# Kernel optimization log

Hardware: AMD Instinct MI355X
Metric: run time of the kernel (lower is better)

The kernel has to match this reference:

```python
import jax, jax.numpy as jnp
import numpy as np

B, D_IN, H, D_OUT = 4096, 64, 128, 512
MAX_STEP = 1000


def setup_inputs() -> dict:
    key = jax.random.key(0)
    ks = jax.random.split(key, 6)
    return {
        "LT": jax.random.uniform(ks[0], (B, D_IN), jnp.float32),
        "K": jax.random.uniform(ks[1], (D_IN, H), jnp.float32),
        "AT": jax.random.uniform(ks[2], (H,), jnp.float32),
        "u": jax.random.uniform(ks[3], (D_IN * H, D_OUT), jnp.float32),
        "e": jax.random.uniform(ks[4], (H, D_OUT), jnp.float32),
        "b": jax.random.uniform(ks[5], (D_OUT,), jnp.float32),
        "max_step": MAX_STEP,
    }


def _st_relu(x):
    # _mask: relu forward, identity backward (straight-through)
    return x + jax.lax.stop_gradient(jax.nn.relu(x) - x)


def _fixed_point(LT, K, AT, max_step):
    # Competitive-binding fixed point. All quantities here are detached in the
    # original (K.detach(), AT.detach()); callers pass stop_gradient'ed values.
    Bn, Din = LT.shape
    Hn = AT.shape[0]
    LTe = LT[:, :, None]            # [B, D_in, 1]
    ATe = AT[:, None]               # [H, 1] broadcasts against [B, H, 1]
    AF0 = jnp.zeros((Bn, Hn, 1), LT.dtype)
    LF0 = jnp.zeros((Bn, Din, 1), LT.dtype)

    def cond(c):
        AF, LF, step, done = c
        return (step < max_step) & (~done)

    def body(c):
        AF, LF, step, _ = c
        Ldi = LTe / (K @ AF + 1.0)            # [B, D_in, 1]
        AF_new = ATe / (K.T @ Ldi + 1.0)      # [B, H, 1]
        Adi = ATe / (K.T @ LF + 1.0)          # [B, H, 1]
        LF_new = LTe / (K @ Adi + 1.0)        # [B, D_in, 1]
        diff = (jnp.abs(AF_new - AF) / (AF + 1e-5)).max() + \
               (jnp.abs(LF_new - LF) / (LF + 1e-5)).max()
        return AF_new, LF_new, step + 1, diff < 1e-3

    AF, LF, _, _ = jax.lax.while_loop(
        cond, body, (AF0, LF0, jnp.int32(0), jnp.array(False)))
    return AF, LF


def reference(LT, K, AT, u, e, b, max_step):
    Km = _st_relu(K)
    ATm = _st_relu(AT)
    sg = jax.lax.stop_gradient
    AF, LF = _fixed_point(sg(LT), sg(Km), sg(ATm), max_step)

    # Final (differentiable) refinement step with undetached params
    LTe = LT[:, :, None]
    ATe = ATm[:, None]
    Ldi = LTe / (Km @ AF + 1.0)
    AF = ATe / (Km.T @ Ldi + 1.0)             # [B, H, 1]
    Adi = ATe / (Km.T @ LF + 1.0)
    LF = LTe / (Km @ Adi + 1.0)               # [B, D_in, 1]

    AFt = jnp.transpose(AF, (0, 2, 1))        # [B, 1, H]
    D = (Km * (LF @ AFt)).reshape(LT.shape[0], -1)  # [B, D_in*H]
    AFs = AFt[:, 0, :]                        # [B, H]
    return D @ u + AFs @ e + b[None, :]       # [B, D_out]
```

## Files before the change

kernel.cpp:

```cpp
#include <hip/hip_runtime.h>

#define B_ROWS 4096
#define DIN 64
#define NH 128
#define DOUT 512
#define ROWS_PER_BLK 16
#define MAXSTEP_CAP 1000

typedef __attribute__((ext_vector_type(8))) short short8;
typedef __attribute__((ext_vector_type(4))) float f32x4;
typedef __attribute__((ext_vector_type(4))) unsigned u32x4;

template<int N> struct IC { static constexpr int v = N; };

__device__ inline unsigned bf16pair(float lo, float hi) {
    unsigned a = __float_as_uint(lo), b = __float_as_uint(hi);
    a = (a + 0x7fffu + ((a >> 16) & 1u)) >> 16;
    b = (b + 0x7fffu + ((b >> 16) & 1u)) >> 16;
    return a | (b << 16);
}
__device__ inline ushort bf16r(float v) {
    unsigned u = __float_as_uint(v);
    return (ushort)((u + 0x7fffu + ((u >> 16) & 1u)) >> 16);
}
__device__ inline float frcp(float x) { return __builtin_amdgcn_rcpf(x); }
__device__ inline short8 as_s8(u32x4 v) { return __builtin_bit_cast(short8, v); }

__device__ inline void splitw(float v, ushort* ph, ushort* pl) {
    unsigned u = __float_as_uint(v);
    unsigned uh = (u + 0x7fffu + ((u >> 16) & 1u)) & 0xffff0000u;
    float rs = v - __uint_as_float(uh);
    unsigned ul = __float_as_uint(rs);
    *ph = (ushort)(uh >> 16);
    *pl = (ushort)((ul + 0x7fffu + ((ul >> 16) & 1u)) >> 16);
}
__device__ inline void packsplit8(const float* x, short8& h8, short8& l8) {
    unsigned hb[8], lb[8];
    #pragma unroll
    for (int j = 0; j < 8; ++j) {
        float v = fmaxf(x[j], 0.0f);
        unsigned u = __float_as_uint(v);
        unsigned uh = (u + 0x7fffu + ((u >> 16) & 1u)) & 0xffff0000u;
        float rs = v - __uint_as_float(uh);
        unsigned ul = __float_as_uint(rs);
        hb[j] = uh >> 16;
        lb[j] = (ul + 0x7fffu + ((ul >> 16) & 1u)) >> 16;
    }
    uint4 hv, lv;
    hv.x = hb[0] | (hb[1] << 16); hv.y = hb[2] | (hb[3] << 16);
    hv.z = hb[4] | (hb[5] << 16); hv.w = hb[6] | (hb[7] << 16);
    lv.x = lb[0] | (lb[1] << 16); lv.y = lb[2] | (lb[3] << 16);
    lv.z = lb[4] | (lb[5] << 16); lv.w = lb[6] | (lb[7] << 16);
    h8 = *reinterpret_cast<short8*>(&hv);
    l8 = *reinterpret_cast<short8*>(&lv);
}

#define ISSUE_SLICE(buf, ptr) do {                                                         \
    const char* _p = (ptr);                                                                \
    asm volatile("global_load_dwordx4 %0, %1, off"             : "=v"(buf[0]) : "v"(_p));  \
    asm volatile("global_load_dwordx4 %0, %1, off offset:1024" : "=v"(buf[1]) : "v"(_p));  \
    asm volatile("global_load_dwordx4 %0, %1, off offset:2048" : "=v"(buf[2]) : "v"(_p));  \
    asm volatile("global_load_dwordx4 %0, %1, off offset:3072" : "=v"(buf[3]) : "v"(_p));  \
} while (0)

#define WAIT_VM(N) do {                                  \
    asm volatile("s_waitcnt vmcnt(" #N ")");             \
    __builtin_amdgcn_sched_barrier(0);                   \
} while (0)

__global__ __launch_bounds__(256, 1)
void solve_chain(const float* __restrict__ LT, const float* __restrict__ Kg,
                 const float* __restrict__ AT, const int* __restrict__ msp,
                 float* __restrict__ AFout, float* __restrict__ LFout)
{
    __shared__ __align__(16) ushort AX[2][16][136];
    __shared__ __align__(16) ushort AY[2][16][136];
    __shared__ __align__(16) ushort LX[2][16][136];
    __shared__ __align__(16) ushort LY[2][16][136];
    __shared__ float wred[4];

    const int tid = threadIdx.x;
    const int lane = tid & 63, w = tid >> 6;
    const int lr = lane & 15, lg = lane >> 4;
    const int b0row = blockIdx.x * ROWS_PER_BLK;

    for (int idx = tid; idx < 2176; idx += 256) {
        reinterpret_cast<unsigned*>(&AX[0][0][0])[idx] = 0u;
        reinterpret_cast<unsigned*>(&LX[0][0][0])[idx] = 0u;
    }

    int max_step = *msp;
    if (max_step > MAXSTEP_CAP) max_step = MAXSTEP_CAP;

    short8 BkH[4], BkL[4];
    #pragma unroll
    for (int ks = 0; ks < 4; ++ks) {
        float xx[8];
        const float* p = &Kg[(16 * w + lr) * NH + ks * 32 + lg * 8];
        #pragma unroll
        for (int j = 0; j < 8; ++j) xx[j] = p[j];
        packsplit8(xx, BkH[ks], BkL[ks]);
    }
    short8 BtH[2][2], BtL[2][2];
    #pragma unroll
    for (int t = 0; t < 2; ++t)
        #pragma unroll
        for (int ks = 0; ks < 2; ++ks) {
            float xx[8];
            #pragma unroll
            for (int j = 0; j < 8; ++j)
                xx[j] = Kg[(ks * 32 + lg * 8 + j) * NH + 32 * w + 16 * t + lr];
            packsplit8(xx, BtH[t][ks], BtL[t][ks]);
        }

    float ltv[4];
    #pragma unroll
    for (int r = 0; r < 4; ++r)
        ltv[r] = LT[(size_t)(b0row + lg * 4 + r) * DIN + 16 * w + lr];
    float atv[2];
    #pragma unroll
    for (int t = 0; t < 2; ++t)
        atv[t] = fmaxf(AT[32 * w + 16 * t + lr], 0.f);

    float prevA[2][4] = {};
    float prevL[4] = {};
    bool done = false;

    __syncthreads();

    auto iterate = [&](auto MC, bool check, float tol) {
        constexpr int mode = decltype(MC)::v;
        {
            f32x4 aH = {0.f,0.f,0.f,0.f}, aL = aH;
            #pragma unroll
            for (int ks = 0; ks < 4; ++ks) {
                short8 hi = *reinterpret_cast<const short8*>(&AX[0][lr][ks * 32 + lg * 8]);
                aH = __builtin_amdgcn_mfma_f32_16x16x32_bf16(hi, BkH[ks], aH, 0, 0, 0);
                if (mode >= 1) {
                    short8 lo = *reinterpret_cast<const short8*>(&AX[1][lr][ks * 32 + lg * 8]);
                    aL = __builtin_amdgcn_mfma_f32_16x16x32_bf16(lo, BkH[ks], aL, 0, 0, 0);
                }
                if (mode == 2)
                    aL = __builtin_amdgcn_mfma_f32_16x16x32_bf16(hi, BkL[ks], aL, 0, 0, 0);
            }
            #pragma unroll
            for (int r = 0; r < 4; ++r) {
                float v = ltv[r] * frcp(aH[r] + aL[r] + 1.0f);
                if (mode == 0) AY[0][lg * 4 + r][16 * w + lr] = bf16r(v);
                else splitw(v, &AY[0][lg * 4 + r][16 * w + lr],
                               &AY[1][lg * 4 + r][16 * w + lr]);
            }
        }
        {
            short8 xh0 = *reinterpret_cast<const short8*>(&LX[0][lr][lg * 8]);
            short8 xh1 = *reinterpret_cast<const short8*>(&LX[0][lr][32 + lg * 8]);
            short8 xl0, xl1;
            if (mode >= 1) {
                xl0 = *reinterpret_cast<const short8*>(&LX[1][lr][lg * 8]);
                xl1 = *reinterpret_cast<const short8*>(&LX[1][lr][32 + lg * 8]);
            }
            #pragma unroll
            for (int t = 0; t < 2; ++t) {
                f32x4 bH = {0.f,0.f,0.f,0.f}, bL = bH;
                bH = __builtin_amdgcn_mfma_f32_16x16x32_bf16(xh0, BtH[t][0], bH, 0, 0, 0);
                bH = __builtin_amdgcn_mfma_f32_16x16x32_bf16(xh1, BtH[t][1], bH, 0, 0, 0);
                if (mode >= 1) {
                    bL = __builtin_amdgcn_mfma_f32_16x16x32_bf16(xl0, BtH[t][0], bL, 0, 0, 0);
                    bL = __builtin_amdgcn_mfma_f32_16x16x32_bf16(xl1, BtH[t][1], bL, 0, 0, 0);
                }
                if (mode == 2) {
                    bL = __builtin_amdgcn_mfma_f32_16x16x32_bf16(xh0, BtL[t][0], bL, 0, 0, 0);
                    bL = __builtin_amdgcn_mfma_f32_16x16x32_bf16(xh1, BtL[t][1], bL, 0, 0, 0);
                }
                #pragma unroll
                for (int r = 0; r < 4; ++r) {
                    float v = atv[t] * frcp(bH[r] + bL[r] + 1.0f);
                    if (mode == 0) LY[0][lg * 4 + r][32 * w + 16 * t + lr] = bf16r(v);
                    else splitw(v, &LY[0][lg * 4 + r][32 * w + 16 * t + lr],
                                   &LY[1][lg * 4 + r][32 * w + 16 * t + lr]);
                }
            }
        }
        __syncthreads();
        float flag = -1.0f;
        {
            short8 yh0 = *reinterpret_cast<const short8*>(&AY[0][lr][lg * 8]);
            short8 yh1 = *reinterpret_cast<const short8*>(&AY[0][lr][32 + lg * 8]);
            short8 yl0, yl1;
            if (mode >= 1) {
                yl0 = *reinterpret_cast<const short8*>(&AY[1][lr][lg * 8]);
                yl1 = *reinterpret_cast<const short8*>(&AY[1][lr][32 + lg * 8]);
            }
            #pragma unroll
            for (int t = 0; t < 2; ++t) {
                f32x4 bH = {0.f,0.f,0.f,0.f}, bL = bH;
                bH = __builtin_amdgcn_mfma_f32_16x16x32_bf16(yh0, BtH[t][0], bH, 0, 0, 0);
                bH = __builtin_amdgcn_mfma_f32_16x16x32_bf16(yh1, BtH[t][1], bH, 0, 0, 0);
                if (mode >= 1) {
                    bL = __builtin_amdgcn_mfma_f32_16x16x32_bf16(yl0, BtH[t][0], bL, 0, 0, 0);
                    bL = __builtin_amdgcn_mfma_f32_16x16x32_bf16(yl1, BtH[t][1], bL, 0, 0, 0);
                }
                if (mode == 2) {
                    bL = __builtin_amdgcn_mfma_f32_16x16x32_bf16(yh0, BtL[t][0], bL, 0, 0, 0);
                    bL = __builtin_amdgcn_mfma_f32_16x16x32_bf16(yh1, BtL[t][1], bL, 0, 0, 0);
                }
                #pragma unroll
                for (int r = 0; r < 4; ++r) {
                    float v = atv[t] * frcp(bH[r] + bL[r] + 1.0f);
                    if (check) {
                        float p = prevA[t][r];
                        flag = fmaxf(flag, fabsf(v - p) - tol * (p + 1e-5f));
                    }
                    prevA[t][r] = v;
                    if (mode == 0) AX[0][lg * 4 + r][32 * w + 16 * t + lr] = bf16r(v);
                    else splitw(v, &AX[0][lg * 4 + r][32 * w + 16 * t + lr],
                                   &AX[1][lg * 4 + r][32 * w + 16 * t + lr]);
                }
            }
        }
        {
            f32x4 aH = {0.f,0.f,0.f,0.f}, aL = aH;
            #pragma unroll
            for (int ks = 0; ks < 4; ++ks) {
                short8 hi = *reinterpret_cast<const short8*>(&LY[0][lr][ks * 32 + lg * 8]);
                aH = __builtin_amdgcn_mfma_f32_16x16x32_bf16(hi, BkH[ks], aH, 0, 0, 0);
                if (mode >= 1) {
                    short8 lo = *reinterpret_cast<const short8*>(&LY[1][lr][ks * 32 + lg * 8]);
                    aL = __builtin_amdgcn_mfma_f32_16x16x32_bf16(lo, BkH[ks], aL, 0, 0, 0);
                }
                if (mode == 2)
                    aL = __builtin_amdgcn_mfma_f32_16x16x32_bf16(hi, BkL[ks], aL, 0, 0, 0);
            }
            #pragma unroll
            for (int r = 0; r < 4; ++r) {
                float v = ltv[r] * frcp(aH[r] + aL[r] + 1.0f);
                if (check) {
                    float p = prevL[r];
                    flag = fmaxf(flag, fabsf(v - p) - tol * (p + 1e-5f));
                }
                prevL[r] = v;
                if (mode == 0) LX[0][lg * 4 + r][16 * w + lr] = bf16r(v);
                else splitw(v, &LX[0][lg * 4 + r][16 * w + lr],
                               &LX[1][lg * 4 + r][16 * w + lr]);
            }
        }
        if (check) {
            #pragma unroll
            for (int off = 32; off; off >>= 1)
                flag = fmaxf(flag, __shfl_xor(flag, off));
            if (lane == 0) wred[w] = flag;
        }
        __syncthreads();
        if (check)
            done = fmaxf(fmaxf(wred[0], wred[1]), fmaxf(wred[2], wred[3])) < 0.0f;
    };

    int step = 0;
    const int cheapN = max_step < 12 ? max_step : 12;
    for (int s = 0; s < cheapN; ++s, ++step)
        iterate(IC<0>{}, false, 0.f);
    const int capC = max_step < 64 ? max_step : 64;
    while (step < capC && !done) { iterate(IC<0>{}, true, 6e-3f); ++step; }
    done = false;
    while (step < max_step && !done) { iterate(IC<1>{}, true, 5e-5f); ++step; }
    iterate(IC<2>{}, false, 0.f);
    iterate(IC<2>{}, false, 0.f);
    iterate(IC<2>{}, false, 0.f);

    #pragma unroll
    for (int t = 0; t < 2; ++t)
        #pragma unroll
        for (int r = 0; r < 4; ++r)
            AFout[(size_t)(b0row + lg * 4 + r) * NH + 32 * w + 16 * t + lr] = prevA[t][r];
    #pragma unroll
    for (int r = 0; r < 4; ++r)
        LFout[(size_t)(b0row + lg * 4 + r) * DIN + 16 * w + lr] = prevL[r];
}

__global__ __launch_bounds__(256, 2)
void prep_wt2(const float* __restrict__ Kg, const float* __restrict__ ug,
              const float* __restrict__ eg, ushort* __restrict__ WT2)
{
    __shared__ float tile[128][68];
    const int t = threadIdx.x;
    const int i = blockIdx.x;
    const int ot = blockIdx.y;
    const int k0 = i * 128;
    const bool mn = (i < 64);

    {
        const int r = t >> 1, c0 = (t & 1) * 32;
        const float* src = mn ? &ug[(size_t)(k0 + r) * DOUT + ot * 64 + c0]
                              : &eg[(size_t)r * DOUT + ot * 64 + c0];
        const float sc = mn ? fmaxf(Kg[k0 + r], 0.0f) : 1.0f;
        #pragma unroll
        for (int g = 0; g < 8; ++g) {
            float4 v = *reinterpret_cast<const float4*>(src + g * 4);
            v.x *= sc; v.y *= sc; v.z *= sc; v.w *= sc;
            *reinterpret_cast<float4*>(&tile[r][c0 + g * 4]) = v;
        }
    }
    __syncthreads();

    {
        const int wnf = t >> 4;
        const int f = wnf & 7;
        const int wn = wnf >> 3;
        const int ks = f & 3, n = (f >> 2) & 1;
        ushort* dst = WT2 + ((size_t)(ot * 65 + i) * 16 + wnf) * 512;
        #pragma unroll
        for (int q = 0; q < 4; ++q) {
            const int l = (t & 15) * 4 + q;
            const int rb = ks * 32 + (l >> 4) * 8;
            const int c  = wn * 32 + n * 16 + (l & 15);
            uint4 v;
            v.x = bf16pair(tile[rb + 0][c], tile[rb + 1][c]);
            v.y = bf16pair(tile[rb + 2][c], tile[rb + 3][c]);
            v.z = bf16pair(tile[rb + 4][c], tile[rb + 5][c]);
            v.w = bf16pair(tile[rb + 6][c], tile[rb + 7][c]);
            *reinterpret_cast<uint4*>(dst + l * 8) = v;
        }
    }
}

__global__ __launch_bounds__(256, 2)
void out_gemm_rank1(const float* __restrict__ AFw, const float* __restrict__ LFw,
                    const ushort* __restrict__ WT2, const float* __restrict__ bg,
                    float* __restrict__ out)
{
    __shared__ __align__(16) ushort AFb[64][136];
    __shared__ __align__(16) float  LFt[64][68];

    const int t = threadIdx.x;
    const int ot = blockIdx.x & 7;
    const int b0 = (blockIdx.x >> 3) * 64, o0 = ot * 64;
    const int w = t >> 6, l = t & 63;
    const int lr = l & 15, lg = l >> 4;

    {
        const int row = t >> 2, q = t & 3;
        const float4* srcA = reinterpret_cast<const float4*>(
            &AFw[(size_t)(b0 + row) * NH + q * 32]);
        #pragma unroll
        for (int g = 0; g < 4; ++g) {
            float4 fa = srcA[2 * g], fb = srcA[2 * g + 1];
            uint4 wv;
            wv.x = bf16pair(fa.x, fa.y); wv.y = bf16pair(fa.z, fa.w);
            wv.z = bf16pair(fb.x, fb.y); wv.w = bf16pair(fb.z, fb.w);
            *reinterpret_cast<uint4*>(&AFb[row][q * 32 + g * 8]) = wv;
        }
        const f32x4* srcL = reinterpret_cast<const f32x4*>(
            &LFw[(size_t)(b0 + row) * DIN + q * 16]);
        #pragma unroll
        for (int g = 0; g < 4; ++g) {
            f32x4 fv = srcL[g];
            #pragma unroll
            for (int j = 0; j < 4; ++j)
                LFt[q * 16 + g * 4 + j][row] = fv[j];
        }
    }
    __syncthreads();

    const char* base = reinterpret_cast<const char*>(WT2)
        + ((size_t)(ot * 65) * 16) * 1024 + w * 4096 + l * 16;

    u32x4 bf0[4], bf1[4], bf2[4];
    ISSUE_SLICE(bf0, base);
    ISSUE_SLICE(bf1, base + 16384);
    ISSUE_SLICE(bf2, base + 2 * 16384);

    short8 afr[4][4];
    #pragma unroll
    for (int m = 0; m < 4; ++m)
        #pragma unroll
        for (int ks = 0; ks < 4; ++ks)
            afr[m][ks] = *reinterpret_cast<const short8*>(
                &AFb[m * 16 + lr][ks * 32 + lg * 8]);

    f32x4 acc[4], tt[4];
    #pragma unroll
    for (int m = 0; m < 4; ++m) acc[m] = (f32x4){0.f, 0.f, 0.f, 0.f};

    auto computeI = [&](const u32x4* bf) {
        #pragma unroll
        for (int m = 0; m < 4; ++m) tt[m] = (f32x4){0.f, 0.f, 0.f, 0.f};
        #pragma unroll
        for (int ks = 0; ks < 4; ++ks) {
            short8 bv = as_s8(bf[ks]);
            #pragma unroll
            for (int m = 0; m < 4; ++m)
                tt[m] = __builtin_amdgcn_mfma_f32_16x16x32_bf16(afr[m][ks], bv, tt[m], 0, 0, 0);
        }
    };
    auto scaleAdd = [&](int i) {
        #pragma unroll
        for (int m = 0; m < 4; ++m) {
            f32x4 lf = *reinterpret_cast<const f32x4*>(&LFt[i][m * 16 + lg * 4]);
            #pragma unroll
            for (int r = 0; r < 4; ++r)
                acc[m][r] += lf[r] * tt[m][r];
        }
    };

    #pragma unroll 1
    for (int i = 0; i < 60; i += 3) {
        const char* p = base + (size_t)(i + 3) * 16384;
        WAIT_VM(8); computeI(bf0); scaleAdd(i);     ISSUE_SLICE(bf0, p);
        WAIT_VM(8); computeI(bf1); scaleAdd(i + 1); ISSUE_SLICE(bf1, p + 16384);
        WAIT_VM(8); computeI(bf2); scaleAdd(i + 2); ISSUE_SLICE(bf2, p + 2 * 16384);
    }
    WAIT_VM(8); computeI(bf0); scaleAdd(60); ISSUE_SLICE(bf0, base + (size_t)63 * 16384);
    WAIT_VM(8); computeI(bf1); scaleAdd(61); ISSUE_SLICE(bf1, base + (size_t)64 * 16384);
    WAIT_VM(8); computeI(bf2); scaleAdd(62);
    WAIT_VM(4); computeI(bf0); scaleAdd(63);
    WAIT_VM(0); computeI(bf1);
    #pragma unroll
    for (int m = 0; m < 4; ++m)
        #pragma unroll
        for (int r = 0; r < 4; ++r)
            acc[m][r] += tt[m][r];

    const int col = o0 + w * 16 + lr;
    const float bb = bg[col];
    #pragma unroll
    for (int m = 0; m < 4; ++m) {
        #pragma unroll
        for (int r = 0; r < 4; ++r) {
            const int row = b0 + m * 16 + lg * 4 + r;
            out[(size_t)row * DOUT + col] = acc[m][r] + bb;
        }
    }
}

extern "C" void kernel_launch(void* const* d_in, const int* in_sizes, int n_in,
                              void* d_out, int out_size, void* d_ws, size_t ws_size,
                              hipStream_t stream)
{
    const float* LT   = (const float*)d_in[0];
    const float* Kg   = (const float*)d_in[1];
    const float* AT   = (const float*)d_in[2];
    const float* ug   = (const float*)d_in[3];
    const float* eg   = (const float*)d_in[4];
    const float* bg   = (const float*)d_in[5];
    const int*   msp  = (const int*)d_in[6];
    float* out = (float*)d_out;

    char* ws = (char*)d_ws;
    float*  AFw = (float*)(ws);
    float*  LFw = (float*)(ws + 2097152);
    ushort* WT2 = (ushort*)(ws + 3145728);

    solve_chain<<<dim3(256), dim3(256), 0, stream>>>(LT, Kg, AT, msp, AFw, LFw);
    prep_wt2<<<dim3(65, 8), dim3(256), 0, stream>>>(Kg, ug, eg, WT2);

    out_gemm_rank1<<<dim3(512), dim3(256), 0, stream>>>(AFw, LFw, WT2, bg, out);
}
```

Before: 76.22 us.

## Fuse weight-prep blocks into solver launch and raise MFMA wave priority

Merges the independent weight-prep kernel into the fixed-point solver launch as extra blocks, sharing a unioned shared-memory buffer. Prep blocks can then run on CUs left idle by the 256 solver blocks instead of waiting in a separate launch. The solver blocks now reserve the larger union of the two LDS layouts, and the prep part inherits the 1-block-per-CU launch bound. Separately, wave priority is raised around the MFMA section of the output GEMM.

```diff
diff --git a/kernel.cpp b/kernel.cpp
--- a/kernel.cpp
+++ b/kernel.cpp
@@ -6,6 +6,7 @@
 #define DOUT 512
 #define ROWS_PER_BLK 16
 #define MAXSTEP_CAP 1000
+#define NBS 256
 
 typedef __attribute__((ext_vector_type(8))) short short8;
 typedef __attribute__((ext_vector_type(4))) float f32x4;
@@ -68,18 +69,76 @@
     __builtin_amdgcn_sched_barrier(0);                   \
 } while (0)
 
+struct SolveSM {
+    ushort AX[2][16][136];
+    ushort AY[2][16][136];
+    ushort LX[2][16][136];
+    ushort LY[2][16][136];
+    float wred[4];
+};
+struct PrepSM {
+    float tile[128][68];
+};
+#define FUSED_SM_BYTES (sizeof(SolveSM) > sizeof(PrepSM) ? sizeof(SolveSM) : sizeof(PrepSM))
+
 __global__ __launch_bounds__(256, 1)
-void solve_chain(const float* __restrict__ LT, const float* __restrict__ Kg,
-                 const float* __restrict__ AT, const int* __restrict__ msp,
-                 float* __restrict__ AFout, float* __restrict__ LFout)
+void solve_prep(const float* __restrict__ LT, const float* __restrict__ Kg,
+                const float* __restrict__ AT, const int* __restrict__ msp,
+                const float* __restrict__ ug, const float* __restrict__ eg,
+                float* __restrict__ AFout, float* __restrict__ LFout,
+                ushort* __restrict__ WT2)
 {
-    __shared__ __align__(16) ushort AX[2][16][136];
-    __shared__ __align__(16) ushort AY[2][16][136];
-    __shared__ __align__(16) ushort LX[2][16][136];
-    __shared__ __align__(16) ushort LY[2][16][136];
-    __shared__ float wred[4];
+    __shared__ __align__(16) unsigned char SMEM[FUSED_SM_BYTES];
 
     const int tid = threadIdx.x;
+
+    if (blockIdx.x >= NBS) {
+        PrepSM& P = *reinterpret_cast<PrepSM*>(SMEM);
+        const int bid2 = blockIdx.x - NBS;
+        const int i = bid2 % 65;
+        const int ot = bid2 / 65;
+        const int k0 = i * 128;
+        const bool mn = (i < 64);
+
+        {
+            const int r = tid >> 1, c0 = (tid & 1) * 32;
+            const float* src = mn ? &ug[(size_t)(k0 + r) * DOUT + ot * 64 + c0]
+                                  : &eg[(size_t)r * DOUT + ot * 64 + c0];
+            const float sc = mn ? fmaxf(Kg[k0 + r], 0.0f) : 1.0f;
+            #pragma unroll
+            for (int g = 0; g < 8; ++g) {
+                float4 v = *reinterpret_cast<const float4*>(src + g * 4);
+                v.x *= sc; v.y *= sc; v.z *= sc; v.w *= sc;
+                *reinterpret_cast<float4*>(&P.tile[r][c0 + g * 4]) = v;
+            }
+        }
+        __syncthreads();
+        {
+            const int wnf = tid >> 4;
+            const int f = wnf & 7;
+            const int wn = wnf >> 3;
+            const int ks = f & 3, n = (f >> 2) & 1;
+            ushort* dst = WT2 + ((size_t)(ot * 65 + i) * 16 + wnf) * 512;
+            #pragma unroll
+            for (int q = 0; q < 4; ++q) {
+                const int l = (tid & 15) * 4 + q;
+                const int rb = ks * 32 + (l >> 4) * 8;
+                const int c  = wn * 32 + n * 16 + (l & 15);
+                uint4 v;
+                v.x = bf16pair(P.tile[rb + 0][c], P.tile[rb + 1][c]);
+                v.y = bf16pair(P.tile[rb + 2][c], P.tile[rb + 3][c]);
+                v.z = bf16pair(P.tile[rb + 4][c], P.tile[rb + 5][c]);
+                v.w = bf16pair(P.tile[rb + 6][c], P.tile[rb + 7][c]);
+                *reinterpret_cast<uint4*>(dst + l * 8) = v;
+            }
+        }
+        return;
+    }
+
+    SolveSM& S = *reinterpret_cast<SolveSM*>(SMEM);
+    auto& AX = S.AX; auto& AY = S.AY; auto& LX = S.LX; auto& LY = S.LY;
+    auto& wred = S.wred;
+
     const int lane = tid & 63, w = tid >> 6;
     const int lr = lane & 15, lg = lane >> 4;
     const int b0row = blockIdx.x * ROWS_PER_BLK;
@@ -278,52 +337,6 @@
 }
 
 __global__ __launch_bounds__(256, 2)
-void prep_wt2(const float* __restrict__ Kg, const float* __restrict__ ug,
-              const float* __restrict__ eg, ushort* __restrict__ WT2)
-{
-    __shared__ float tile[128][68];
-    const int t = threadIdx.x;
-    const int i = blockIdx.x;
-    const int ot = blockIdx.y;
-    const int k0 = i * 128;
-    const bool mn = (i < 64);
-
-    {
-        const int r = t >> 1, c0 = (t & 1) * 32;
-        const float* src = mn ? &ug[(size_t)(k0 + r) * DOUT + ot * 64 + c0]
-                              : &eg[(size_t)r * DOUT + ot * 64 + c0];
-        const float sc = mn ? fmaxf(Kg[k0 + r], 0.0f) : 1.0f;
-        #pragma unroll
-        for (int g = 0; g < 8; ++g) {
-            float4 v = *reinterpret_cast<const float4*>(src + g * 4);
-            v.x *= sc; v.y *= sc; v.z *= sc; v.w *= sc;
-            *reinterpret_cast<float4*>(&tile[r][c0 + g * 4]) = v;
-        }
-    }
-    __syncthreads();
-
-    {
-        const int wnf = t >> 4;
-        const int f = wnf & 7;
-        const int wn = wnf >> 3;
-        const int ks = f & 3, n = (f >> 2) & 1;
-        ushort* dst = WT2 + ((size_t)(ot * 65 + i) * 16 + wnf) * 512;
-        #pragma unroll
-        for (int q = 0; q < 4; ++q) {
-            const int l = (t & 15) * 4 + q;
-            const int rb = ks * 32 + (l >> 4) * 8;
-            const int c  = wn * 32 + n * 16 + (l & 15);
-            uint4 v;
-            v.x = bf16pair(tile[rb + 0][c], tile[rb + 1][c]);
-            v.y = bf16pair(tile[rb + 2][c], tile[rb + 3][c]);
-            v.z = bf16pair(tile[rb + 4][c], tile[rb + 5][c]);
-            v.w = bf16pair(tile[rb + 6][c], tile[rb + 7][c]);
-            *reinterpret_cast<uint4*>(dst + l * 8) = v;
-        }
-    }
-}
-
-__global__ __launch_bounds__(256, 2)
 void out_gemm_rank1(const float* __restrict__ AFw, const float* __restrict__ LFw,
                     const ushort* __restrict__ WT2, const float* __restrict__ bg,
                     float* __restrict__ out)
@@ -384,6 +397,7 @@
     auto computeI = [&](const u32x4* bf) {
         #pragma unroll
         for (int m = 0; m < 4; ++m) tt[m] = (f32x4){0.f, 0.f, 0.f, 0.f};
+        __builtin_amdgcn_s_setprio(1);
         #pragma unroll
         for (int ks = 0; ks < 4; ++ks) {
             short8 bv = as_s8(bf[ks]);
@@ -391,6 +405,7 @@
             for (int m = 0; m < 4; ++m)
                 tt[m] = __builtin_amdgcn_mfma_f32_16x16x32_bf16(afr[m][ks], bv, tt[m], 0, 0, 0);
         }
+        __builtin_amdgcn_s_setprio(0);
     };
     auto scaleAdd = [&](int i) {
         #pragma unroll
@@ -450,8 +465,8 @@
     float*  LFw = (float*)(ws + 2097152);
     ushort* WT2 = (ushort*)(ws + 3145728);
 
-    solve_chain<<<dim3(256), dim3(256), 0, stream>>>(LT, Kg, AT, msp, AFw, LFw);
-    prep_wt2<<<dim3(65, 8), dim3(256), 0, stream>>>(Kg, ug, eg, WT2);
+    solve_prep<<<dim3(NBS + 520), dim3(256), 0, stream>>>(
+        LT, Kg, AT, msp, ug, eg, AFw, LFw, WT2);
 
     out_gemm_rank1<<<dim3(512), dim3(256), 0, stream>>>(AFw, LFw, WT2, bg, out);
 }
```

Result: faster. 69.51 us (-8.8%).
